# Kernel tuning notes

Measured on AMD Instinct MI355X. Metric: run time of the kernel, lower is better.

Reference implementation:

```python
import jax, jax.numpy as jnp
import numpy as np

NEG_INF = jnp.float32(-1e30)
EPS = 1e-7  # keras.backend.ctc_batch_cost epsilon


def ctc_batch_cost(y_true, y_pred):
    """Faithful CTC loss (keras ctc_batch_cost semantics): y_pred are
    probabilities [B,T,C], blank = C-1, full input/label lengths.
    Returns per-example negative log likelihood [B,1]."""
    B, T, C = y_pred.shape
    L = y_true.shape[1]
    S = 2 * L + 1  # extended label length (blanks interleaved)
    blank = C - 1

    log_probs = jnp.log(y_pred + EPS)  # [B,T,C]

    # Extended label sequence: blank, l0, blank, l1, ..., blank  -> [B,S]
    ext = jnp.full((B, S), blank, dtype=y_true.dtype)
    ext = ext.at[:, 1::2].set(y_true)

    # Skip transition allowed at s if ext[s] != blank and ext[s] != ext[s-2]
    skip = jnp.concatenate(
        [jnp.zeros((B, 2), dtype=bool),
         (ext[:, 2:] != blank) & (ext[:, 2:] != ext[:, :-2])], axis=1)  # [B,S]

    # Gather log-probs of extended labels per timestep: [T,B,S]
    lp_ext = jnp.take_along_axis(log_probs, ext[:, None, :], axis=2)  # [B,T,S]
    lp_ext = jnp.transpose(lp_ext, (1, 0, 2))  # [T,B,S]

    # alpha init at t=0: only positions 0 (blank) and 1 (first label)
    alpha0 = jnp.full((B, S), NEG_INF, dtype=log_probs.dtype)
    alpha0 = alpha0.at[:, 0].set(lp_ext[0, :, 0])
    alpha0 = alpha0.at[:, 1].set(lp_ext[0, :, 1])

    pad1 = jnp.full((B, 1), NEG_INF, dtype=log_probs.dtype)
    pad2 = jnp.full((B, 2), NEG_INF, dtype=log_probs.dtype)

    def step(alpha, lp_t):
        a_stay = alpha
        a_prev = jnp.concatenate([pad1, alpha[:, :-1]], axis=1)
        a_skip = jnp.where(skip, jnp.concatenate([pad2, alpha[:, :-2]], axis=1), NEG_INF)
        m = jnp.maximum(jnp.maximum(a_stay, a_prev), a_skip)
        lse = m + jnp.log(jnp.exp(a_stay - m) + jnp.exp(a_prev - m) + jnp.exp(a_skip - m))
        return lse + lp_t, None

    alpha_T, _ = jax.lax.scan(step, alpha0, lp_ext[1:])  # [B,S]

    # log P = logsumexp over last blank and last label positions
    end = jnp.stack([alpha_T[:, S - 1], alpha_T[:, S - 2]], axis=1)  # [B,2]
    loglik = jax.nn.logsumexp(end, axis=1)  # [B]
    return -loglik[:, None]  # [B,1] like keras ctc_batch_cost


def setup_inputs() -> dict:
    key = jax.random.key(0)
    k1, k2 = jax.random.split(key)
    B, T, C, L = 512, 512, 128, 32
    y_true = jax.random.randint(k1, (B, L), 0, C - 1, dtype=jnp.int64 if jax.config.read('jax_enable_x64') else jnp.int32)
    y_pred = jax.random.uniform(k2, (B, T, C), dtype=jnp.float32)
    return {"y_true": y_true, "y_pred": y_pred}


def reference(y_true, y_pred):
    return ctc_batch_cost(y_true, y_pred)
```

## Files before the change

kernel.cpp:

```cpp
#include <hip/hip_runtime.h>


#define EPSF 1e-7f

constexpr int T_   = 512;
constexpr int C_   = 128;
constexpr int L_   = 32;
constexpr int NG   = 127;
constexpr int NLD  = 17;
constexpr int NBUF = 16;

static_assert(NG == 127, "");

__device__ __forceinline__ void gl16(const float* gp, float* lp) {
    __builtin_amdgcn_global_load_lds(
        (const __attribute__((address_space(1))) void*)gp,
        (__attribute__((address_space(3))) void*)lp,
        16, 0, 0);
}

__device__ __forceinline__ float wshr1(float x) {
    return __int_as_float(
        __builtin_amdgcn_mov_dpp(__float_as_int(x), 0x138, 0xf, 0xf, true));
}

__launch_bounds__(64)
__global__ void ctc_loss_kernel(const int* __restrict__ y_true,
                                const float* __restrict__ y_pred,
                                float* __restrict__ out) {
    __shared__ float smem[NBUF * 512];

    const int b    = blockIdx.x;
    const int lane = threadIdx.x;

    const float* bb  = y_pred + (size_t)b * T_ * C_;
    const int*   lbl = y_true + b * L_;

    int   cls[7];
    float sg[7];
#pragma unroll
    for (int i = 0; i < 7; ++i) {
        const int v = lane - i;
        int   c = C_ - 1;
        float s = 0.f;
        if (v >= 1 && (v & 1)) {
            c = lbl[(v - 1) >> 1];
            if (v >= 3 && c != lbl[((v - 1) >> 1) - 1]) s = 1.f;
        }
        cls[i] = c;
        sg[i]  = s;
    }

    float a       = (lane < 2) ? (bb[cls[0]] + EPSF) : 0.f;
    float a64     = 0.f;
    int   e_total = 0;

    auto issueG = [&](int g) {
        const float* src = bb + (size_t)(1 + 4 * g) * C_ + lane * 4;
        float* dst = &smem[(g & (NBUF - 1)) * 512];
        gl16(src,       dst);
        gl16(src + 256, dst + 256);
    };

    auto ldsq = [&](float (&Qk)[NLD], int g) {
        const float* r = &smem[(g & (NBUF - 1)) * 512];
        Qk[0]  = r[cls[0]];          Qk[1]  = r[cls[1]];
        Qk[2]  = r[cls[2]];          Qk[3]  = r[cls[3]];
        Qk[4]  = r[cls[4]];          Qk[5]  = r[cls[5]];
        Qk[6]  = r[cls[6]];
        Qk[7]  = r[C_ + cls[0]];     Qk[8]  = r[C_ + cls[1]];
        Qk[9]  = r[C_ + cls[2]];     Qk[10] = r[C_ + cls[3]];
        Qk[11] = r[C_ + cls[4]];
        Qk[12] = r[2 * C_ + cls[0]]; Qk[13] = r[2 * C_ + cls[1]];
        Qk[14] = r[2 * C_ + cls[2]];
        Qk[15] = r[3 * C_ + cls[0]]; Qk[16] = r[3 * C_ + cls[1]];
    };

    auto sample_eb = [&]() -> int {
        int mb = __builtin_amdgcn_readlane(__float_as_int(a), 3);
#pragma unroll
        for (int i = 1; i < 16; ++i) {
            const int v = __builtin_amdgcn_readlane(__float_as_int(a), 4 * i + 3);
            mb = (v > mb) ? v : mb;
        }
        const int eb = (int)((unsigned)mb >> 23);
        return (eb > 27) ? eb : 27;
    };

    auto apply_scale = [&](int eb) {
        e_total += eb - 127;
        const float inv = __uint_as_float((unsigned)(254 - eb) << 23);
        a   *= inv;
        a64 *= inv;
    };

    auto group4 = [&](float (&Qk)[NLD]) {
        float A[9];
        A[0] = a;
#pragma unroll
        for (int i = 1; i <= 8; ++i) A[i] = wshr1(A[i - 1]);

        float B[7];
#pragma unroll
        for (int i = 0; i <= 6; ++i)
            B[i] = (A[i] + A[i + 1] + sg[i] * A[i + 2]) * (Qk[i] + EPSF);
        float Cc[5];
#pragma unroll
        for (int i = 0; i <= 4; ++i)
            Cc[i] = (B[i] + B[i + 1] + sg[i] * B[i + 2]) * (Qk[7 + i] + EPSF);
        float D[3];
#pragma unroll
        for (int i = 0; i <= 2; ++i)
            D[i] = (Cc[i] + Cc[i + 1] + sg[i] * Cc[i + 2]) * (Qk[12 + i] + EPSF);

        float z = a64;
        z = (z + A[0])  * (Qk[1]  + EPSF);
        z = (z + B[0])  * (Qk[8]  + EPSF);
        z = (z + Cc[0]) * (Qk[13] + EPSF);
        z = (z + D[0])  * (Qk[16] + EPSF);
        a64 = z;

        a = (D[0] + D[1] + sg[0] * D[2]) * (Qk[15] + EPSF);
    };

    int ebp = sample_eb();

#pragma unroll
    for (int k = 0; k < 15; ++k) issueG(k);
    asm volatile("s_waitcnt vmcnt(28)" ::: "memory");

    float QA[NLD], QB[NLD];
    ldsq(QA, 0);

    for (int g0 = 0; g0 < 112; g0 += 2) {
        issueG(g0 + 15);
        asm volatile("s_waitcnt vmcnt(28)" ::: "memory");
        ldsq(QB, g0 + 1);
        group4(QA);
        apply_scale(ebp);
        ebp = sample_eb();

        issueG(g0 + 16);
        asm volatile("s_waitcnt vmcnt(28)" ::: "memory");
        ldsq(QA, g0 + 2);
        group4(QB);
        apply_scale(ebp);
        ebp = sample_eb();
    }

    float qo[3], qb2[3];
#pragma unroll
    for (int r = 0; r < 3; ++r) {
        const float* rp = bb + (size_t)(509 + r) * C_;
        qo[r]  = rp[cls[0]];
        qb2[r] = rp[cls[1]];
    }

    asm volatile("s_waitcnt vmcnt(0)" ::: "memory");

    for (int g0 = 112; g0 < 126; g0 += 2) {
        ldsq(QB, g0 + 1);
        group4(QA);
        apply_scale(ebp);
        ebp = sample_eb();
        ldsq(QA, g0 + 2);
        group4(QB);
        apply_scale(ebp);
        ebp = sample_eb();
    }
    group4(QA);
    apply_scale(ebp);

#pragma unroll
    for (int r = 0; r < 3; ++r) {
        const float p1 = wshr1(a);
        const float p2 = wshr1(p1);
        const float anew = (a + p1 + sg[0] * p2) * (qo[r] + EPSF);
        a64 = (a64 + a) * (qb2[r] + EPSF);
        a = anew;
    }

    if (lane == 63) {
        out[b] = -(__logf(a + a64) + (float)e_total * 0.6931471805599453f);
    }
}

extern "C" void kernel_launch(void* const* d_in, const int* in_sizes, int n_in,
                              void* d_out, int out_size, void* d_ws, size_t ws_size,
                              hipStream_t stream) {
    const int*   y_true = (const int*)d_in[0];
    const float* y_pred = (const float*)d_in[1];
    float*       out    = (float*)d_out;

    const int B = out_size;
    ctc_loss_kernel<<<B, 64, 0, stream>>>(y_true, y_pred, out);
}
```

Measured before the change: 198.0 us.

## Replace LDS staging with direct register gathers and DPP lane shifts

Drops the global-to-LDS async copy ring buffer and the 17 LDS gathers per 4-step group. Each lane now loads only its own class probability per timestep straight from global memory into registers, with an 8-group register prefetch. The values for neighbouring lanes (cls[i] = class of lane-i) come from DPP row shifts instead of extra LDS reads. This cuts LDS traffic and instruction count but adds DPP ops on the critical path. It also relies on plain scattered global loads, whose latency is hidden only by the register prefetch depth.

```diff
diff --git a/kernel.cpp b/kernel.cpp
--- a/kernel.cpp
+++ b/kernel.cpp
@@ -3,21 +3,11 @@
 
 #define EPSF 1e-7f
 
-constexpr int T_   = 512;
-constexpr int C_   = 128;
-constexpr int L_   = 32;
-constexpr int NG   = 127;
-constexpr int NLD  = 17;
-constexpr int NBUF = 16;
-
-static_assert(NG == 127, "");
-
-__device__ __forceinline__ void gl16(const float* gp, float* lp) {
-    __builtin_amdgcn_global_load_lds(
-        (const __attribute__((address_space(1))) void*)gp,
-        (__attribute__((address_space(3))) void*)lp,
-        16, 0, 0);
-}
+constexpr int T_  = 512;
+constexpr int C_  = 128;
+constexpr int L_  = 32;
+constexpr int NG  = 127;
+constexpr int PFG = 8;
 
 __device__ __forceinline__ float wshr1(float x) {
     return __int_as_float(
@@ -28,52 +18,40 @@
 __global__ void ctc_loss_kernel(const int* __restrict__ y_true,
                                 const float* __restrict__ y_pred,
                                 float* __restrict__ out) {
-    __shared__ float smem[NBUF * 512];
-
     const int b    = blockIdx.x;
     const int lane = threadIdx.x;
 
     const float* bb  = y_pred + (size_t)b * T_ * C_;
     const int*   lbl = y_true + b * L_;
 
-    int   cls[7];
+    int   cls0;
     float sg[7];
+    {
+        int c0 = C_ - 1;
+        if (lane >= 1 && (lane & 1)) c0 = lbl[(lane - 1) >> 1];
+        cls0 = c0;
 #pragma unroll
-    for (int i = 0; i < 7; ++i) {
-        const int v = lane - i;
-        int   c = C_ - 1;
-        float s = 0.f;
-        if (v >= 1 && (v & 1)) {
-            c = lbl[(v - 1) >> 1];
-            if (v >= 3 && c != lbl[((v - 1) >> 1) - 1]) s = 1.f;
+        for (int i = 0; i < 7; ++i) {
+            const int v = lane - i;
+            float s = 0.f;
+            if (v >= 3 && (v & 1)) {
+                const int c = lbl[(v - 1) >> 1];
+                if (c != lbl[((v - 1) >> 1) - 1]) s = 1.f;
+            }
+            sg[i] = s;
         }
-        cls[i] = c;
-        sg[i]  = s;
     }
 
-    float a       = (lane < 2) ? (bb[cls[0]] + EPSF) : 0.f;
+    float a       = (lane < 2) ? (bb[cls0] + EPSF) : 0.f;
     float a64     = 0.f;
     int   e_total = 0;
 
-    auto issueG = [&](int g) {
-        const float* src = bb + (size_t)(1 + 4 * g) * C_ + lane * 4;
-        float* dst = &smem[(g & (NBUF - 1)) * 512];
-        gl16(src,       dst);
-        gl16(src + 256, dst + 256);
-    };
-
-    auto ldsq = [&](float (&Qk)[NLD], int g) {
-        const float* r = &smem[(g & (NBUF - 1)) * 512];
-        Qk[0]  = r[cls[0]];          Qk[1]  = r[cls[1]];
-        Qk[2]  = r[cls[2]];          Qk[3]  = r[cls[3]];
-        Qk[4]  = r[cls[4]];          Qk[5]  = r[cls[5]];
-        Qk[6]  = r[cls[6]];
-        Qk[7]  = r[C_ + cls[0]];     Qk[8]  = r[C_ + cls[1]];
-        Qk[9]  = r[C_ + cls[2]];     Qk[10] = r[C_ + cls[3]];
-        Qk[11] = r[C_ + cls[4]];
-        Qk[12] = r[2 * C_ + cls[0]]; Qk[13] = r[2 * C_ + cls[1]];
-        Qk[14] = r[2 * C_ + cls[2]];
-        Qk[15] = r[3 * C_ + cls[0]]; Qk[16] = r[3 * C_ + cls[1]];
+    auto loadQ = [&](float (&Pk)[4], int g) {
+        const float* r = bb + (size_t)(1 + 4 * g) * C_ + cls0;
+        Pk[0] = r[0];
+        Pk[1] = r[C_];
+        Pk[2] = r[2 * C_];
+        Pk[3] = r[3 * C_];
     };
 
     auto sample_eb = [&]() -> int {
@@ -94,7 +72,23 @@
         a64 *= inv;
     };
 
-    auto group4 = [&](float (&Qk)[NLD]) {
+    auto group4 = [&](const float (&P)[4]) {
+        float q0[7];
+        q0[0] = P[0] + EPSF;
+#pragma unroll
+        for (int i = 1; i < 7; ++i) q0[i] = wshr1(q0[i - 1]);
+        float q1[5];
+        q1[0] = P[1] + EPSF;
+#pragma unroll
+        for (int i = 1; i < 5; ++i) q1[i] = wshr1(q1[i - 1]);
+        float q2[3];
+        q2[0] = P[2] + EPSF;
+#pragma unroll
+        for (int i = 1; i < 3; ++i) q2[i] = wshr1(q2[i - 1]);
+        float q3[2];
+        q3[0] = P[3] + EPSF;
+        q3[1] = wshr1(q3[0]);
+
         float A[9];
         A[0] = a;
 #pragma unroll
@@ -103,80 +97,68 @@
         float B[7];
 #pragma unroll
         for (int i = 0; i <= 6; ++i)
-            B[i] = (A[i] + A[i + 1] + sg[i] * A[i + 2]) * (Qk[i] + EPSF);
+            B[i] = (A[i] + A[i + 1] + sg[i] * A[i + 2]) * q0[i];
         float Cc[5];
 #pragma unroll
         for (int i = 0; i <= 4; ++i)
-            Cc[i] = (B[i] + B[i + 1] + sg[i] * B[i + 2]) * (Qk[7 + i] + EPSF);
+            Cc[i] = (B[i] + B[i + 1] + sg[i] * B[i + 2]) * q1[i];
         float D[3];
 #pragma unroll
         for (int i = 0; i <= 2; ++i)
-            D[i] = (Cc[i] + Cc[i + 1] + sg[i] * Cc[i + 2]) * (Qk[12 + i] + EPSF);
+            D[i] = (Cc[i] + Cc[i + 1] + sg[i] * Cc[i + 2]) * q2[i];
 
         float z = a64;
-        z = (z + A[0])  * (Qk[1]  + EPSF);
-        z = (z + B[0])  * (Qk[8]  + EPSF);
-        z = (z + Cc[0]) * (Qk[13] + EPSF);
-        z = (z + D[0])  * (Qk[16] + EPSF);
+        z = (z + A[0])  * q0[1];
+        z = (z + B[0])  * q1[1];
+        z = (z + Cc[0]) * q2[1];
+        z = (z + D[0])  * q3[1];
         a64 = z;
 
-        a = (D[0] + D[1] + sg[0] * D[2]) * (Qk[15] + EPSF);
+        a = (D[0] + D[1] + sg[0] * D[2]) * q3[0];
     };
+
+    float Q[PFG][4];
+#pragma unroll
+    for (int k = 0; k < PFG; ++k) loadQ(Q[k], k);
 
     int ebp = sample_eb();
 
+    for (int g0 = 0; g0 < 112; g0 += PFG) {
 #pragma unroll
-    for (int k = 0; k < 15; ++k) issueG(k);
-    asm volatile("s_waitcnt vmcnt(28)" ::: "memory");
+        for (int k = 0; k < PFG; ++k) {
+            group4(Q[k]);
+            apply_scale(ebp);
+            ebp = sample_eb();
+            loadQ(Q[k], g0 + k + PFG);
+        }
+    }
 
-    float QA[NLD], QB[NLD];
-    ldsq(QA, 0);
-
-    for (int g0 = 0; g0 < 112; g0 += 2) {
-        issueG(g0 + 15);
-        asm volatile("s_waitcnt vmcnt(28)" ::: "memory");
-        ldsq(QB, g0 + 1);
-        group4(QA);
+#pragma unroll
+    for (int k = 0; k < PFG; ++k) {
+        group4(Q[k]);
         apply_scale(ebp);
         ebp = sample_eb();
-
-        issueG(g0 + 16);
-        asm volatile("s_waitcnt vmcnt(28)" ::: "memory");
-        ldsq(QA, g0 + 2);
-        group4(QB);
-        apply_scale(ebp);
-        ebp = sample_eb();
+        if (k < 7) loadQ(Q[k], 120 + k);
     }
 
-    float qo[3], qb2[3];
+    float qo[3];
 #pragma unroll
-    for (int r = 0; r < 3; ++r) {
-        const float* rp = bb + (size_t)(509 + r) * C_;
-        qo[r]  = rp[cls[0]];
-        qb2[r] = rp[cls[1]];
+    for (int r = 0; r < 3; ++r) qo[r] = bb[(size_t)(509 + r) * C_ + cls0];
+
+#pragma unroll
+    for (int k = 0; k < 7; ++k) {
+        group4(Q[k]);
+        apply_scale(ebp);
+        if (k < 6) ebp = sample_eb();
     }
-
-    asm volatile("s_waitcnt vmcnt(0)" ::: "memory");
-
-    for (int g0 = 112; g0 < 126; g0 += 2) {
-        ldsq(QB, g0 + 1);
-        group4(QA);
-        apply_scale(ebp);
-        ebp = sample_eb();
-        ldsq(QA, g0 + 2);
-        group4(QB);
-        apply_scale(ebp);
-        ebp = sample_eb();
-    }
-    group4(QA);
-    apply_scale(ebp);
 
 #pragma unroll
     for (int r = 0; r < 3; ++r) {
         const float p1 = wshr1(a);
         const float p2 = wshr1(p1);
+        const float qb = wshr1(qo[r]);
         const float anew = (a + p1 + sg[0] * p2) * (qo[r] + EPSF);
-        a64 = (a64 + a) * (qb2[r] + EPSF);
+        a64 = (a64 + a) * (qb + EPSF);
         a = anew;
     }
 
```

After: 203.2 us. +2.6%, slower.
